# Kernel optimization log

Measured on AMD Instinct MI355X. Metric: run time of the kernel, lower is better.

## Reference

```python
import jax, jax.numpy as jnp
import numpy as np

DIM = 384
HEADS = 8


def conv1x1(x, w):
    # x: [b,c,h,w], w: [o,c] (1x1 conv, no bias)
    return jnp.einsum('bchw,oc->bohw', x, w)


def dwconv3x3(x, w):
    # depthwise 3x3, padding=1. x: [b,c,h,w], w: [c,1,3,3]
    return jax.lax.conv_general_dilated(
        x, w, window_strides=(1, 1), padding='SAME',
        feature_group_count=x.shape[1],
        dimension_numbers=('NCHW', 'OIHW', 'NCHW'))


def l2norm(x, eps=1e-12):
    # F.normalize(dim=-1): x / max(||x||_2, eps)
    n = jnp.sqrt(jnp.sum(x * x, axis=-1, keepdims=True))
    return x / jnp.maximum(n, eps)


def topm_softmax(attn, m):
    # keep top-m per row (by value threshold == scatter of topk indices), -inf elsewhere
    thr = jax.lax.top_k(attn, m)[0][..., -1:]
    return jax.nn.softmax(jnp.where(attn >= thr, attn, -jnp.inf), axis=-1)


def setup_inputs() -> dict:
    key = jax.random.key(0)
    ks = jax.random.split(key, 9)
    d = DIM
    return {
        'x_q': jax.random.normal(ks[0], (8, d, 128, 128), jnp.float32),
        'x_kv': jax.random.normal(ks[1], (8, d, 128, 128), jnp.float32),
        'q_w': jax.random.normal(ks[2], (d, d), jnp.float32) * 0.02,
        'q_dw': jax.random.normal(ks[3], (d, 1, 3, 3), jnp.float32) * 0.02,
        'kv_w': jax.random.normal(ks[4], (2 * d, d), jnp.float32) * 0.02,
        'kv_dw': jax.random.normal(ks[5], (2 * d, 1, 3, 3), jnp.float32) * 0.02,
        'proj_w': jax.random.normal(ks[6], (d, d), jnp.float32) * 0.02,
        'temperature': jnp.ones((HEADS, 1, 1), jnp.float32),
        'a_mix': jnp.full((4,), 0.2, jnp.float32),  # attn1..attn4
    }


def reference(x_q, x_kv, q_w, q_dw, kv_w, kv_dw, proj_w, temperature, a_mix):
    b, c, h, w = x_q.shape
    C = c // HEADS  # channels per head
    n = h * w

    q = dwconv3x3(conv1x1(x_q, q_w), q_dw)
    kv = dwconv3x3(conv1x1(x_kv, kv_w), kv_dw)
    k, v = jnp.split(kv, 2, axis=1)

    q = l2norm(q.reshape(b, HEADS, C, n))
    k = l2norm(k.reshape(b, HEADS, C, n))
    v = v.reshape(b, HEADS, C, n)

    attn = jnp.einsum('bhcn,bhdn->bhcd', q, k) * temperature  # [b,H,C,C]

    topks = (C // 2, (2 * C) // 3, (3 * C) // 4, (4 * C) // 5)
    out = jnp.zeros_like(v)
    for i, m in enumerate(topks):
        a = topm_softmax(attn, m)
        out = out + a_mix[i] * jnp.einsum('bhcd,bhdn->bhcn', a, v)

    out = out.reshape(b, c, h, w)
    return conv1x1(out, proj_w)
```

## Files before the change

kernel.cpp:

```cpp
#include <hip/hip_runtime.h>
#include <cstdint>
#include <cstddef>

#define DIM 384
#define HEADS 8
#define NBATCH 8
#define NPIX 16384
#define CPH 48

typedef unsigned short h16_t;
typedef __attribute__((ext_vector_type(8))) _Float16 half8;
typedef __attribute__((ext_vector_type(4))) float floatx4;

#define VM_WAIT(n) asm volatile("s_waitcnt vmcnt(" #n ")" ::: "memory")
#define LGKM_WAIT0 asm volatile("s_waitcnt lgkmcnt(0)" ::: "memory")

__device__ __forceinline__ h16_t f2h(float f) {
  _Float16 h = (_Float16)f;
  return __builtin_bit_cast(h16_t, h);
}
__device__ __forceinline__ float h2f(h16_t u) {
  return (float)__builtin_bit_cast(_Float16, u);
}

__device__ __forceinline__ void gload_lds16(const void* g, void* l) {
  __builtin_amdgcn_global_load_lds(
      (const __attribute__((address_space(1))) unsigned int*)g,
      (__attribute__((address_space(3))) unsigned int*)l, 16, 0, 0);
}

__global__ void convert_h16_kernel(const float* __restrict__ in, h16_t* __restrict__ out, int n) {
  int i = blockIdx.x * blockDim.x + threadIdx.x;
  if (i < n) out[i] = f2h(in[i]);
}

template <bool F32OUT, bool ABATCH, typename BT>
__global__ __launch_bounds__(256, 3) void gemm_tn_kernel(
    const h16_t* __restrict__ Aall, const BT* __restrict__ Ball, void* __restrict__ Cout) {
  __shared__ __align__(16) h16_t lA[2][128 * 64];
  __shared__ __align__(16) h16_t lB[128 * 72];
  int b = blockIdx.z, mb = blockIdx.y, nb = blockIdx.x;
  const h16_t* A = Aall + (ABATCH ? (size_t)b * DIM * DIM : (size_t)0) + (size_t)mb * 128 * DIM;
  const BT* B = Ball + (size_t)b * DIM * NPIX + (size_t)nb * 128;
  int tid = threadIdx.x;
  int wid = tid >> 6, lane = tid & 63;
  int wi = wid >> 1, wj = wid & 1;
  int quad = lane >> 4, l15 = lane & 15;
  int srow = lane >> 3;
  int schunk = (lane & 7) ^ srow;
  int koct = tid & 7;
  int n4 = tid >> 3;

  float4 f[8];
  ushort4 u[8];
  auto loadB = [&](int ktL) {
    const BT* bp = B + (size_t)(ktL * 64 + koct * 8) * NPIX + (size_t)n4 * 4;
#pragma unroll
    for (int i = 0; i < 8; ++i) {
      if constexpr (sizeof(BT) == 4)
        f[i] = *(const float4*)(bp + (size_t)i * NPIX);
      else
        u[i] = *(const ushort4*)(bp + (size_t)i * NPIX);
    }
  };
  auto stageA = [&](int ktL, int buf) {
#pragma unroll
    for (int t = 0; t < 4; ++t) {
      int r = (wid * 4 + t) * 8 + srow;
      gload_lds16(A + (size_t)r * DIM + ktL * 64 + schunk * 8,
                  (char*)&lA[buf][0] + (wid * 4 + t) * 1024 + lane * 16);
    }
  };

  floatx4 acc[4][4];
#pragma unroll
  for (int i = 0; i < 4; ++i)
#pragma unroll
    for (int j = 0; j < 4; ++j) acc[i][j] = (floatx4)0.0f;

  stageA(0, 0);
  loadB(0);

#pragma unroll
  for (int kt = 0; kt < 6; ++kt) {
    const int c = kt & 1;
    if (kt < 5) stageA(kt + 1, 1 - c);
    if (kt < 5) { VM_WAIT(4); } else { VM_WAIT(0); }
    __builtin_amdgcn_sched_barrier(0);
    half8 w0, w1, w2, w3;
#pragma unroll
    for (int i = 0; i < 8; ++i) {
      if constexpr (sizeof(BT) == 4) {
        w0[i] = (_Float16)f[i].x; w1[i] = (_Float16)f[i].y;
        w2[i] = (_Float16)f[i].z; w3[i] = (_Float16)f[i].w;
      } else {
        w0[i] = __builtin_bit_cast(_Float16, u[i].x);
        w1[i] = __builtin_bit_cast(_Float16, u[i].y);
        w2[i] = __builtin_bit_cast(_Float16, u[i].z);
        w3[i] = __builtin_bit_cast(_Float16, u[i].w);
      }
    }
    {
      char* bb = (char*)lB + n4 * (4 * 144) + koct * 16;
      *(half8*)(bb + 0)   = w0;
      *(half8*)(bb + 144) = w1;
      *(half8*)(bb + 288) = w2;
      *(half8*)(bb + 432) = w3;
    }
    if (kt < 5) loadB(kt + 1);
    LGKM_WAIT0;
    __builtin_amdgcn_sched_barrier(0);
    __builtin_amdgcn_s_barrier();
#pragma unroll
    for (int ks = 0; ks < 2; ++ks) {
      half8 af[4], bfr[4];
      int ph = (((ks << 2) | quad) ^ (l15 & 7)) << 4;
      int pb = (((ks << 2) | quad)) << 4;
#pragma unroll
      for (int i = 0; i < 4; ++i)
        af[i] = *(const half8*)((const char*)&lA[c][0] + (wi * 64 + i * 16 + l15) * 128 + ph);
#pragma unroll
      for (int j = 0; j < 4; ++j)
        bfr[j] = *(const half8*)((const char*)lB + (wj * 64 + j * 16 + l15) * 144 + pb);
#pragma unroll
      for (int i = 0; i < 4; ++i)
#pragma unroll
        for (int j = 0; j < 4; ++j)
          acc[i][j] = __builtin_amdgcn_mfma_f32_16x16x32_f16(af[i], bfr[j], acc[i][j], 0, 0, 0);
    }
    LGKM_WAIT0;
    __builtin_amdgcn_sched_barrier(0);
    __builtin_amdgcn_s_barrier();
  }
  int orow0 = mb * 128 + wi * 64 + quad * 4;
  int ncol0 = nb * 128 + wj * 64 + l15;
#pragma unroll
  for (int i = 0; i < 4; ++i) {
#pragma unroll
    for (int j = 0; j < 4; ++j) {
#pragma unroll
      for (int r = 0; r < 4; ++r) {
        size_t idx = ((size_t)b * DIM + (orow0 + i * 16 + r)) * NPIX + (ncol0 + j * 16);
        if (F32OUT)
          ((float*)Cout)[idx] = acc[i][j][r];
        else
          ((h16_t*)Cout)[idx] = f2h(acc[i][j][r]);
      }
    }
  }
}

__device__ __forceinline__ void load_row6(const h16_t* ip, int yy, int x0, float* r) {
  if ((unsigned)yy > 127u) {
    r[0] = r[1] = r[2] = r[3] = r[4] = r[5] = 0.f;
    return;
  }
  const h16_t* row = ip + (yy << 7) + x0;
  ushort4 m = *(const ushort4*)row;
  r[0] = (x0 > 0) ? h2f(row[-1]) : 0.f;
  r[1] = h2f(m.x); r[2] = h2f(m.y); r[3] = h2f(m.z); r[4] = h2f(m.w);
  r[5] = (x0 < 124) ? h2f(row[4]) : 0.f;
}

__global__ __launch_bounds__(256) void dwconv_kernel(
    const h16_t* __restrict__ in, const float* __restrict__ wbase,
    h16_t* __restrict__ out, float* __restrict__ norm2) {
  int c = blockIdx.x, b = blockIdx.y;
  const h16_t* ip = in + ((size_t)(b * DIM + c) << 14);
  h16_t* op = out + ((size_t)(b * DIM + c) << 14);
  const float* wp = wbase + c * 9;
  float w0 = wp[0], w1 = wp[1], w2 = wp[2], w3 = wp[3], w4 = wp[4];
  float w5 = wp[5], w6 = wp[6], w7 = wp[7], w8 = wp[8];
  float ssum = 0.f;
  for (int t = threadIdx.x; t < 4096; t += 256) {
    int y = t >> 5;
    int x0 = (t & 31) << 2;
    float r0[6], r1[6], r2[6];
    load_row6(ip, y - 1, x0, r0);
    load_row6(ip, y,     x0, r1);
    load_row6(ip, y + 1, x0, r2);
    ushort4 st;
#pragma unroll
    for (int i = 0; i < 4; ++i) {
      float o = w0 * r0[i] + w1 * r0[i + 1] + w2 * r0[i + 2]
              + w3 * r1[i] + w4 * r1[i + 1] + w5 * r1[i + 2]
              + w6 * r2[i] + w7 * r2[i + 1] + w8 * r2[i + 2];
      h16_t ob = f2h(o);
      float of = h2f(ob);
      ssum += of * of;
      if (i == 0) st.x = ob; else if (i == 1) st.y = ob; else if (i == 2) st.z = ob; else st.w = ob;
    }
    *(ushort4*)(op + (y << 7) + x0) = st;
  }
  if (norm2 != nullptr) {
    __shared__ float red[256];
    int tid = threadIdx.x;
    red[tid] = ssum;
    __syncthreads();
    for (int s = 128; s > 0; s >>= 1) {
      if (tid < s) red[tid] += red[tid + s];
      __syncthreads();
    }
    if (tid == 0) norm2[b * DIM + c] = red[0];
  }
}

__global__ __launch_bounds__(64) void attn_gemm_kernel(
    const h16_t* __restrict__ q, const h16_t* __restrict__ k, float* __restrict__ attn) {
  int chunk = blockIdx.x, bh = blockIdx.y;
  int b = bh >> 3, h = bh & 7;
  const h16_t* qb = q + ((size_t)(b * DIM + h * CPH) << 14);
  const h16_t* kb = k + ((size_t)(b * DIM + h * CPH) << 14);
  int lane = threadIdx.x;
  int quad = lane >> 4, l15 = lane & 15;
  int off0 = chunk * 1024 + quad * 8;
  floatx4 acc[3][3];
#pragma unroll
  for (int i = 0; i < 3; ++i)
#pragma unroll
    for (int j = 0; j < 3; ++j) acc[i][j] = (floatx4)0.0f;
  for (int s = 0; s < 32; ++s) {
    int off = off0 + s * 32;
    half8 af[3], bfr[3];
#pragma unroll
    for (int i = 0; i < 3; ++i) {
      af[i]  = *(const half8*)(qb + ((size_t)(i * 16 + l15) << 14) + off);
      bfr[i] = *(const half8*)(kb + ((size_t)(i * 16 + l15) << 14) + off);
    }
#pragma unroll
    for (int i = 0; i < 3; ++i)
#pragma unroll
      for (int j = 0; j < 3; ++j)
        acc[i][j] = __builtin_amdgcn_mfma_f32_16x16x32_f16(af[i], bfr[j], acc[i][j], 0, 0, 0);
  }
  float* ap = attn + (size_t)bh * CPH * CPH;
#pragma unroll
  for (int i = 0; i < 3; ++i)
#pragma unroll
    for (int j = 0; j < 3; ++j)
#pragma unroll
      for (int r = 0; r < 4; ++r)
        atomicAdd(&ap[(i * 16 + quad * 4 + r) * CPH + j * 16 + l15], acc[i][j][r]);
}

__global__ __launch_bounds__(256) void combine_kernel(
    const float* __restrict__ attn, const float* __restrict__ n2q, const float* __restrict__ n2k,
    const float* __restrict__ temp, const float* __restrict__ amix,
    const float* __restrict__ projw, h16_t* __restrict__ Bmat) {
  int bh = blockIdx.x;
  int b = bh >> 3, h = bh & 7;
  __shared__ float Asc[CPH][CPH];
  __shared__ float Ex[CPH][CPH];
  __shared__ float thr[CPH][4];
  __shared__ float rmax[CPH];
  __shared__ float den[CPH][4];
  __shared__ float rsq[CPH], rsk[CPH];
  int tid = threadIdx.x;
  if (tid < CPH) {
    float nq = sqrtf(n2q[b * DIM + h * CPH + tid]);
    rsq[tid] = 1.f / fmaxf(nq, 1e-12f);
    float nk = sqrtf(n2k[b * DIM + h * CPH + tid]);
    rsk[tid] = 1.f / fmaxf(nk, 1e-12f);
  }
  __syncthreads();
  float tscale = temp[h];
  const float* ap = attn + (size_t)bh * CPH * CPH;
  for (int idx = tid; idx < CPH * CPH; idx += 256) {
    int c = idx / CPH, d = idx - c * CPH;
    Asc[c][d] = ap[idx] * rsq[c] * rsk[d] * tscale;
  }
  __syncthreads();
  const int M0 = 24, M1 = 32, M2 = 36, M3 = 38;
  for (int idx = tid; idx < CPH * CPH; idx += 256) {
    int c = idx / CPH, d = idx - c * CPH;
    float a = Asc[c][d];
    int gt = 0, ge = 0;
    float mx = -1e30f;
    for (int e = 0; e < CPH; ++e) {
      float v = Asc[c][e];
      gt += (v > a);
      ge += (v >= a);
      mx = fmaxf(mx, v);
    }
    if (d == 0) rmax[c] = mx;
    if (gt < M0 && ge >= M0) thr[c][0] = a;
    if (gt < M1 && ge >= M1) thr[c][1] = a;
    if (gt < M2 && ge >= M2) thr[c][2] = a;
    if (gt < M3 && ge >= M3) thr[c][3] = a;
  }
  __syncthreads();
  for (int idx = tid; idx < CPH * CPH; idx += 256) {
    int c = idx / CPH, d = idx - c * CPH;
    Ex[c][d] = expf(Asc[c][d] - rmax[c]);
  }
  __syncthreads();
  if (tid < CPH * 4) {
    int c = tid >> 2, mi = tid & 3;
    float t_ = thr[c][mi];
    float s = 0.f;
    for (int e = 0; e < CPH; ++e)
      if (Asc[c][e] >= t_) s += Ex[c][e];
    den[c][mi] = s;
  }
  __syncthreads();
  float a0 = amix[0], a1 = amix[1], a2 = amix[2], a3 = amix[3];
  for (int idx = tid; idx < CPH * CPH; idx += 256) {
    int c = idx / CPH, d = idx - c * CPH;
    float a = Asc[c][d];
    float s = 0.f;
    if (a >= thr[c][0]) s += a0 / den[c][0];
    if (a >= thr[c][1]) s += a1 / den[c][1];
    if (a >= thr[c][2]) s += a2 / den[c][2];
    if (a >= thr[c][3]) s += a3 / den[c][3];
    Ex[c][d] = Ex[c][d] * s;
  }
  __syncthreads();
  for (int idx = tid; idx < DIM * CPH; idx += 256) {
    int o = idx / CPH, d = idx - (idx / CPH) * CPH;
    const float* pw = projw + (size_t)o * DIM + h * CPH;
    float s = 0.f;
    for (int c2 = 0; c2 < CPH; ++c2) s += pw[c2] * Ex[c2][d];
    Bmat[((size_t)b * DIM + o) * DIM + h * CPH + d] = f2h(s);
  }
}

extern "C" void kernel_launch(void* const* d_in, const int* in_sizes, int n_in,
                              void* d_out, int out_size, void* d_ws, size_t ws_size,
                              hipStream_t stream) {
  const float* x_q    = (const float*)d_in[0];
  const float* x_kv   = (const float*)d_in[1];
  const float* q_w    = (const float*)d_in[2];
  const float* q_dw   = (const float*)d_in[3];
  const float* kv_w   = (const float*)d_in[4];
  const float* kv_dw  = (const float*)d_in[5];
  const float* proj_w = (const float*)d_in[6];
  const float* temp   = (const float*)d_in[7];
  const float* amix   = (const float*)d_in[8];

  char* ws = (char*)d_ws;
  const size_t SLOT = (size_t)NBATCH * NPIX * DIM * 2;
  h16_t* S0 = (h16_t*)(ws);
  h16_t* S1 = (h16_t*)(ws + SLOT);
  h16_t* S2 = (h16_t*)(ws + 2 * SLOT);
  h16_t* S3 = (h16_t*)(ws + 3 * SLOT);
  char* p = ws + 4 * SLOT;
  h16_t* WqB  = (h16_t*)p; p += (size_t)DIM * DIM * 2;
  h16_t* WkvB = (h16_t*)p; p += (size_t)2 * DIM * DIM * 2;
  float* n2q  = (float*)p;  p += (size_t)NBATCH * DIM * 4;
  float* n2k  = (float*)p;  p += (size_t)NBATCH * DIM * 4;
  float* attn = (float*)p;  p += (size_t)64 * CPH * CPH * 4;
  h16_t* Bmat = (h16_t*)p; p += (size_t)NBATCH * DIM * DIM * 2;

  hipMemsetAsync(attn, 0, (size_t)64 * CPH * CPH * 4, stream);

  convert_h16_kernel<<<dim3((DIM * DIM + 255) / 256), 256, 0, stream>>>(q_w, WqB, DIM * DIM);
  convert_h16_kernel<<<dim3((2 * DIM * DIM + 255) / 256), 256, 0, stream>>>(kv_w, WkvB, 2 * DIM * DIM);

  dim3 ggrid(NPIX / 128, DIM / 128, NBATCH);

  gemm_tn_kernel<false, false, float><<<ggrid, 256, 0, stream>>>(WqB, x_q, S0);
  dwconv_kernel<<<dim3(DIM, NBATCH), 256, 0, stream>>>(S0, q_dw, S2, n2q);

  gemm_tn_kernel<false, false, float><<<ggrid, 256, 0, stream>>>(WkvB, x_kv, S0);
  gemm_tn_kernel<false, false, float><<<ggrid, 256, 0, stream>>>(WkvB + (size_t)DIM * DIM, x_kv, S1);
  dwconv_kernel<<<dim3(DIM, NBATCH), 256, 0, stream>>>(S0, kv_dw, S3, n2k);

  attn_gemm_kernel<<<dim3(16, 64), 64, 0, stream>>>(S2, S3, attn);
  combine_kernel<<<dim3(64), 256, 0, stream>>>(attn, n2q, n2k, temp, amix, proj_w, Bmat);

  dwconv_kernel<<<dim3(DIM, NBATCH), 256, 0, stream>>>(S1, kv_dw + (size_t)DIM * 9, S2, nullptr);

  gemm_tn_kernel<true, true, h16_t><<<ggrid, 256, 0, stream>>>(Bmat, S2, d_out);
}
```

Measured before the change: 1.208 ms.

## Stage full-K activation panel in LDS and loop over all output row blocks

Replaces the 128x128-tile GEMM with a panel kernel. Each block loads a 64-column slab of B covering all 384 K rows into LDS once, converting it to fp16 on the way. It then streams the weight matrix A through double-buffered LDS for every M block. This stops B (the large activation, read as fp32 for the input convs) from being re-read once per M block, and merges the two kv GEMMs into one launch that writes to two outputs. The costs are larger LDS use (48KB for B plus 32KB for A), lower occupancy (launch bound 2), smaller per-wave N tiles, and fewer blocks in the grid.

```diff
diff --git a/kernel.cpp b/kernel.cpp
--- a/kernel.cpp
+++ b/kernel.cpp
@@ -1,6 +1,7 @@
 #include <hip/hip_runtime.h>
 #include <cstdint>
 #include <cstddef>
+#include <type_traits>
 
 #define DIM 384
 #define HEADS 8
@@ -34,119 +35,148 @@
   if (i < n) out[i] = f2h(in[i]);
 }
 
-template <bool F32OUT, bool ABATCH, typename BT>
-__global__ __launch_bounds__(256, 3) void gemm_tn_kernel(
-    const h16_t* __restrict__ Aall, const BT* __restrict__ Ball, void* __restrict__ Cout) {
+template <int MBLKS, bool SPLIT, bool F32OUT, bool ABATCH, typename BT>
+__global__ __launch_bounds__(256, 2) void gemm_panel_kernel(
+    const h16_t* __restrict__ Aall, const BT* __restrict__ Ball,
+    void* __restrict__ C0, void* __restrict__ C1) {
+  __shared__ __align__(16) h16_t lB[64 * 384];
   __shared__ __align__(16) h16_t lA[2][128 * 64];
-  __shared__ __align__(16) h16_t lB[128 * 72];
-  int b = blockIdx.z, mb = blockIdx.y, nb = blockIdx.x;
-  const h16_t* A = Aall + (ABATCH ? (size_t)b * DIM * DIM : (size_t)0) + (size_t)mb * 128 * DIM;
-  const BT* B = Ball + (size_t)b * DIM * NPIX + (size_t)nb * 128;
+  constexpr int NP = MBLKS * 6;
+  int b = blockIdx.y, nb = blockIdx.x;
+  const h16_t* A = Aall + (ABATCH ? (size_t)b * (MBLKS * 128) * DIM : (size_t)0);
+  const BT* B = Ball + (size_t)b * DIM * NPIX + (size_t)nb * 64;
   int tid = threadIdx.x;
   int wid = tid >> 6, lane = tid & 63;
-  int wi = wid >> 1, wj = wid & 1;
+  int wm = wid >> 1, wn = wid & 1;
   int quad = lane >> 4, l15 = lane & 15;
   int srow = lane >> 3;
   int schunk = (lane & 7) ^ srow;
-  int koct = tid & 7;
-  int n4 = tid >> 3;
-
-  float4 f[8];
-  ushort4 u[8];
-  auto loadB = [&](int ktL) {
-    const BT* bp = B + (size_t)(ktL * 64 + koct * 8) * NPIX + (size_t)n4 * 4;
+  int rgrp = tid >> 4;
+  int n4 = tid & 15;
+
+  using VT = typename std::conditional<sizeof(BT) == 4, float4, ushort4>::type;
+  VT va[8], vb[8];
+
+  auto loadStep = [&](int s, VT* arr) {
+    const BT* bp = B + (size_t)(s * 128 + rgrp * 8) * NPIX + n4 * 4;
+#pragma unroll
+    for (int i = 0; i < 8; ++i) arr[i] = *(const VT*)(bp + (size_t)i * NPIX);
+  };
+  auto writeStep = [&](int s, VT* arr) {
+    half8 w0, w1, w2, w3;
 #pragma unroll
     for (int i = 0; i < 8; ++i) {
-      if constexpr (sizeof(BT) == 4)
-        f[i] = *(const float4*)(bp + (size_t)i * NPIX);
-      else
-        u[i] = *(const ushort4*)(bp + (size_t)i * NPIX);
+      if constexpr (sizeof(BT) == 4) {
+        w0[i] = (_Float16)arr[i].x; w1[i] = (_Float16)arr[i].y;
+        w2[i] = (_Float16)arr[i].z; w3[i] = (_Float16)arr[i].w;
+      } else {
+        w0[i] = __builtin_bit_cast(_Float16, arr[i].x);
+        w1[i] = __builtin_bit_cast(_Float16, arr[i].y);
+        w2[i] = __builtin_bit_cast(_Float16, arr[i].z);
+        w3[i] = __builtin_bit_cast(_Float16, arr[i].w);
+      }
+    }
+    int chunk = s * 16 + rgrp;
+#pragma unroll
+    for (int j = 0; j < 4; ++j) {
+      int n = n4 * 4 + j;
+      int phys = chunk ^ (n & 7);
+      half8* d = (half8*)((char*)lB + n * 768 + phys * 16);
+      *d = (j == 0) ? w0 : (j == 1) ? w1 : (j == 2) ? w2 : w3;
     }
   };
-  auto stageA = [&](int ktL, int buf) {
+  auto stageA = [&](int p, int buf) {
+    int mbn = p / 6, ktn = p - mbn * 6;
+    const h16_t* base = A + (size_t)mbn * 128 * DIM + ktn * 64;
 #pragma unroll
     for (int t = 0; t < 4; ++t) {
       int r = (wid * 4 + t) * 8 + srow;
-      gload_lds16(A + (size_t)r * DIM + ktL * 64 + schunk * 8,
+      gload_lds16(base + (size_t)r * DIM + schunk * 8,
                   (char*)&lA[buf][0] + (wid * 4 + t) * 1024 + lane * 16);
     }
   };
 
-  floatx4 acc[4][4];
-#pragma unroll
-  for (int i = 0; i < 4; ++i)
-#pragma unroll
-    for (int j = 0; j < 4; ++j) acc[i][j] = (floatx4)0.0f;
-
   stageA(0, 0);
-  loadB(0);
-
-#pragma unroll
-  for (int kt = 0; kt < 6; ++kt) {
-    const int c = kt & 1;
-    if (kt < 5) stageA(kt + 1, 1 - c);
-    if (kt < 5) { VM_WAIT(4); } else { VM_WAIT(0); }
+  loadStep(0, va);
+  loadStep(1, vb);
+  VM_WAIT(8);
+  __builtin_amdgcn_sched_barrier(0);
+  writeStep(0, va);
+  loadStep(2, va);
+  VM_WAIT(8);
+  __builtin_amdgcn_sched_barrier(0);
+  writeStep(1, vb);
+  VM_WAIT(0);
+  __builtin_amdgcn_sched_barrier(0);
+  writeStep(2, va);
+  LGKM_WAIT0;
+  __builtin_amdgcn_sched_barrier(0);
+  __builtin_amdgcn_s_barrier();
+
+  floatx4 acc[4][2];
+  int pb = 0;
+  for (int p = 0; p < NP; ++p) {
+    int mb = p / 6, kt = p - mb * 6;
+    if (p + 1 < NP) {
+      stageA(p + 1, pb ^ 1);
+      VM_WAIT(4);
+    } else {
+      VM_WAIT(0);
+    }
     __builtin_amdgcn_sched_barrier(0);
-    half8 w0, w1, w2, w3;
-#pragma unroll
-    for (int i = 0; i < 8; ++i) {
-      if constexpr (sizeof(BT) == 4) {
-        w0[i] = (_Float16)f[i].x; w1[i] = (_Float16)f[i].y;
-        w2[i] = (_Float16)f[i].z; w3[i] = (_Float16)f[i].w;
-      } else {
-        w0[i] = __builtin_bit_cast(_Float16, u[i].x);
-        w1[i] = __builtin_bit_cast(_Float16, u[i].y);
-        w2[i] = __builtin_bit_cast(_Float16, u[i].z);
-        w3[i] = __builtin_bit_cast(_Float16, u[i].w);
+    __builtin_amdgcn_s_barrier();
+    if (kt == 0) {
+#pragma unroll
+      for (int i = 0; i < 4; ++i)
+#pragma unroll
+        for (int j = 0; j < 2; ++j) acc[i][j] = (floatx4)0.0f;
+    }
+    const char* la = (const char*)&lA[pb][0];
+#pragma unroll
+    for (int ks = 0; ks < 2; ++ks) {
+      half8 af[4], bfr[2];
+      int ph = (((ks << 2) | quad) ^ (l15 & 7)) << 4;
+#pragma unroll
+      for (int i = 0; i < 4; ++i)
+        af[i] = *(const half8*)(la + (wm * 64 + i * 16 + l15) * 128 + ph);
+#pragma unroll
+      for (int j = 0; j < 2; ++j) {
+        int n = wn * 32 + j * 16 + l15;
+        int phys = (kt * 8 + ks * 4 + quad) ^ (l15 & 7);
+        bfr[j] = *(const half8*)((const char*)lB + n * 768 + phys * 16);
       }
-    }
-    {
-      char* bb = (char*)lB + n4 * (4 * 144) + koct * 16;
-      *(half8*)(bb + 0)   = w0;
-      *(half8*)(bb + 144) = w1;
-      *(half8*)(bb + 288) = w2;
-      *(half8*)(bb + 432) = w3;
-    }
-    if (kt < 5) loadB(kt + 1);
+#pragma unroll
+      for (int i = 0; i < 4; ++i)
+#pragma unroll
+        for (int j = 0; j < 2; ++j)
+          acc[i][j] = __builtin_amdgcn_mfma_f32_16x16x32_f16(af[i], bfr[j], acc[i][j], 0, 0, 0);
+    }
+    if (kt == 5) {
+      int orow0 = mb * 128 + wm * 64 + quad * 4;
+      int ncol0 = nb * 64 + wn * 32 + l15;
+      char* dst;
+      int m0;
+      if (SPLIT && mb >= 3) { dst = (char*)C1; m0 = orow0 - 384; }
+      else                  { dst = (char*)C0; m0 = orow0; }
+#pragma unroll
+      for (int i = 0; i < 4; ++i) {
+#pragma unroll
+        for (int j = 0; j < 2; ++j) {
+#pragma unroll
+          for (int r = 0; r < 4; ++r) {
+            size_t idx = ((size_t)b * DIM + (m0 + i * 16 + r)) * NPIX + (ncol0 + j * 16);
+            if (F32OUT)
+              ((float*)dst)[idx] = acc[i][j][r];
+            else
+              ((h16_t*)dst)[idx] = f2h(acc[i][j][r]);
+          }
+        }
+      }
+    }
     LGKM_WAIT0;
     __builtin_amdgcn_sched_barrier(0);
     __builtin_amdgcn_s_barrier();
-#pragma unroll
-    for (int ks = 0; ks < 2; ++ks) {
-      half8 af[4], bfr[4];
-      int ph = (((ks << 2) | quad) ^ (l15 & 7)) << 4;
-      int pb = (((ks << 2) | quad)) << 4;
-#pragma unroll
-      for (int i = 0; i < 4; ++i)
-        af[i] = *(const half8*)((const char*)&lA[c][0] + (wi * 64 + i * 16 + l15) * 128 + ph);
-#pragma unroll
-      for (int j = 0; j < 4; ++j)
-        bfr[j] = *(const half8*)((const char*)lB + (wj * 64 + j * 16 + l15) * 144 + pb);
-#pragma unroll
-      for (int i = 0; i < 4; ++i)
-#pragma unroll
-        for (int j = 0; j < 4; ++j)
-          acc[i][j] = __builtin_amdgcn_mfma_f32_16x16x32_f16(af[i], bfr[j], acc[i][j], 0, 0, 0);
-    }
-    LGKM_WAIT0;
-    __builtin_amdgcn_sched_barrier(0);
-    __builtin_amdgcn_s_barrier();
-  }
-  int orow0 = mb * 128 + wi * 64 + quad * 4;
-  int ncol0 = nb * 128 + wj * 64 + l15;
-#pragma unroll
-  for (int i = 0; i < 4; ++i) {
-#pragma unroll
-    for (int j = 0; j < 4; ++j) {
-#pragma unroll
-      for (int r = 0; r < 4; ++r) {
-        size_t idx = ((size_t)b * DIM + (orow0 + i * 16 + r)) * NPIX + (ncol0 + j * 16);
-        if (F32OUT)
-          ((float*)Cout)[idx] = acc[i][j][r];
-        else
-          ((h16_t*)Cout)[idx] = f2h(acc[i][j][r]);
-      }
-    }
+    pb ^= 1;
   }
 }
 
@@ -356,13 +386,12 @@
   convert_h16_kernel<<<dim3((DIM * DIM + 255) / 256), 256, 0, stream>>>(q_w, WqB, DIM * DIM);
   convert_h16_kernel<<<dim3((2 * DIM * DIM + 255) / 256), 256, 0, stream>>>(kv_w, WkvB, 2 * DIM * DIM);
 
-  dim3 ggrid(NPIX / 128, DIM / 128, NBATCH);
-
-  gemm_tn_kernel<false, false, float><<<ggrid, 256, 0, stream>>>(WqB, x_q, S0);
+  dim3 pgrid(NPIX / 64, NBATCH);
+
+  gemm_panel_kernel<3, false, false, false, float><<<pgrid, 256, 0, stream>>>(WqB, x_q, S0, nullptr);
   dwconv_kernel<<<dim3(DIM, NBATCH), 256, 0, stream>>>(S0, q_dw, S2, n2q);
 
-  gemm_tn_kernel<false, false, float><<<ggrid, 256, 0, stream>>>(WkvB, x_kv, S0);
-  gemm_tn_kernel<false, false, float><<<ggrid, 256, 0, stream>>>(WkvB + (size_t)DIM * DIM, x_kv, S1);
+  gemm_panel_kernel<6, true, false, false, float><<<pgrid, 256, 0, stream>>>(WkvB, x_kv, S0, S1);
   dwconv_kernel<<<dim3(DIM, NBATCH), 256, 0, stream>>>(S0, kv_dw, S3, n2k);
 
   attn_gemm_kernel<<<dim3(16, 64), 64, 0, stream>>>(S2, S3, attn);
@@ -370,5 +399,5 @@
 
   dwconv_kernel<<<dim3(DIM, NBATCH), 256, 0, stream>>>(S1, kv_dw + (size_t)DIM * 9, S2, nullptr);
 
-  gemm_tn_kernel<true, true, h16_t><<<ggrid, 256, 0, stream>>>(Bmat, S2, d_out);
-}
+  gemm_panel_kernel<3, false, true, true, h16_t><<<pgrid, 256, 0, stream>>>(Bmat, S2, d_out, nullptr);
+}
```

Measured after the change: 1.192 ms. No clear change (-1.3%).
